# Performance work log

Measured on AMD Instinct MI355X. Metric: run time of the kernel, lower is better.

## Reference

```python
import jax, jax.numpy as jnp
import numpy as np

B, N_CLS, M_TIME, U_LAB = 1024, 96, 256, 40


def setup_inputs() -> dict:
    key = jax.random.key(0)
    k1, k2, k3 = jax.random.split(key, 3)
    logits = jax.random.normal(k1, (B, N_CLS, M_TIME), dtype=jnp.float32)
    # module treats inputs as per-timestep class probabilities (softmax output of CRNN)
    out_padded = jax.nn.softmax(logits, axis=1)
    label = jax.random.randint(k2, (B, U_LAB), 1, N_CLS, dtype=jnp.int32)  # 0 is blank
    unpadded_w = jax.random.randint(k3, (B,), 512, 4 * M_TIME + 1, dtype=jnp.int32)
    return {"out_padded": out_padded, "label": label, "unpadded_w": unpadded_w}


def _alpha(probs, lab, T, L):
    # probs: (M, N) time-major class probabilities; lab: (U,) label indices; T traced int.
    # Faithful to compute_alpha: per-timestep renormalization over [start, end),
    # recurrence computed for s in [start, L).
    M = probs.shape[0]
    s_idx = jnp.arange(L)
    i_idx = jnp.maximum((s_idx - 1) // 2, 0)
    is_odd = (s_idx % 2) == 1
    cls = jnp.where(is_odd, lab[i_idx], 0)  # blank = class 0 for even s
    # skip (a[t-1][s-2]) allowed only for odd s != 1 with non-repeated label
    skip = is_odd & (s_idx != 1) & (lab[i_idx] != lab[jnp.maximum(i_idx - 1, 0)])

    p0 = probs[0]
    row0 = jnp.zeros((L,), probs.dtype).at[0].set(p0[0]).at[1].set(p0[lab[0]])
    c0 = row0[0] + row0[1]
    row0 = jnp.where((s_idx < 2) & (c0 > 0), row0 / jnp.where(c0 > 0, c0, 1.0), row0)

    def step(prev, t):
        start = jnp.maximum(0, L - 2 * (T - t))
        end = jnp.minimum(2 * t + 2, L)
        pm1 = jnp.concatenate([jnp.zeros((1,), prev.dtype), prev[:-1]])
        pm2 = jnp.concatenate([jnp.zeros((2,), prev.dtype), prev[:-2]])
        val = (prev
               + jnp.where(s_idx > 0, pm1, 0.0)
               + jnp.where(skip, pm2, 0.0)) * probs[t, cls]
        val = jnp.where(s_idx >= start, val, 0.0)  # s < start stays zero
        nmask = (s_idx >= start) & (s_idx < end)
        c = jnp.sum(jnp.where(nmask, val, 0.0))
        val = jnp.where(nmask & (c > 0), val / jnp.where(c > 0, c, 1.0), val)
        return val, val

    _, rows = jax.lax.scan(step, row0, jnp.arange(1, M))
    a = jnp.concatenate([row0[None, :], rows], axis=0)  # (M, L)
    return jnp.where((jnp.arange(M) < T)[:, None], a, 0.0)  # rows >= T are zero


def _ctc_single(out_cw, lab, w):
    probs = out_cw.T  # (M, N): time x classes, as in torch.transpose(out, 1, 0)
    M = probs.shape[0]
    U = lab.shape[0]
    L = 2 * U + 1
    T = w // 4
    a = _alpha(probs, lab, T, L)
    # 'beta' faithful to source: alpha on CLASS-flipped probs (torch.fliplr on (T,N))
    # with reversed labels, then flipud+fliplr of the (T,L) result.
    b_raw = _alpha(probs[:, ::-1], lab[::-1], T, L)
    src = T - 1 - jnp.arange(M)
    valid = (src >= 0) & (src < M)
    b = jnp.where(valid[:, None], b_raw[jnp.clip(src, 0, M - 1)], 0.0)[:, ::-1]
    ab = a * b  # (M, L)
    s_idx = jnp.arange(L)
    cls = jnp.where((s_idx % 2) == 1, lab[jnp.maximum((s_idx - 1) // 2, 0)], 0)
    lh = jnp.sum(ab / probs[:, cls], axis=1)  # (M,)
    tmask = jnp.arange(M) < T
    return -jnp.sum(jnp.where(tmask, jnp.log(jnp.where(tmask, lh, 1.0)), 0.0))


def reference(out_padded, label, unpadded_w):
    losses = jax.vmap(_ctc_single)(out_padded, label, unpadded_w)  # (B,)
    return jnp.sum(losses)
```

## Files before the change

kernel.cpp:

```cpp
#include <hip/hip_runtime.h>
#include <cmath>

namespace {
constexpr int BN = 1024;
constexpr int NC = 96;
constexpr int MT = 256;
constexpr int UL = 40;
constexpr int LS = 81;
constexpr int PAIRS = 41;
constexpr int ROWS = 128;

template <int CTRL>
__device__ __forceinline__ float dppf(float v) {
  return __builtin_bit_cast(
      float, __builtin_amdgcn_update_dpp(0, __builtin_bit_cast(int, v), CTRL,
                                         0xf, 0xf, true));
}
__device__ __forceinline__ float rl63(float x) {
  return __builtin_bit_cast(
      float, __builtin_amdgcn_readlane(__builtin_bit_cast(int, x), 63));
}
__device__ __forceinline__ float wave_sum(float x) {
  x += dppf<0x111>(x);
  x += dppf<0x112>(x);
  x += dppf<0x114>(x);
  x += dppf<0x118>(x);
  x += dppf<0x142>(x);
  x += dppf<0x143>(x);
  return rl63(x);
}
__device__ __forceinline__ float wave_shr1(float v) { return dppf<0x138>(v); }
__device__ __forceinline__ float fast_rcp(float x) {
  return __builtin_amdgcn_rcpf(x);
}
__device__ __forceinline__ unsigned packu(float a, float b) {
  unsigned ua = __builtin_bit_cast(unsigned, a) >> 16;
  unsigned ub = __builtin_bit_cast(unsigned, b) & 0xffff0000u;
  return ua | ub;
}
__device__ __forceinline__ float bf_lo(unsigned u) {
  return __builtin_bit_cast(float, u << 16);
}
__device__ __forceinline__ float bf_hi(unsigned u) {
  return __builtin_bit_cast(float, u & 0xffff0000u);
}

constexpr float FQ = 1e8f;
constexpr float SEPS = 1e-30f;

__global__ __launch_bounds__(128) void ctc_fused_kernel(
    const float* __restrict__ gout, const int* __restrict__ glabel,
    const int* __restrict__ gw, float* __restrict__ loss_out) {
  __shared__ unsigned srows[2][ROWS * PAIRS];
  __shared__ float spart[2];
  const int b = blockIdx.x;
  const int ph = threadIdx.x >> 6;
  const int i = threadIdx.x & 63;
  const float* P = gout + (size_t)b * (NC * MT);
  const int* lab = glabel + b * UL;
  const int T = gw[b] >> 2;

  const int s0 = 2 * i, s1 = s0 + 1;
  const float h0f = (i <= 40) ? 1.f : 0.f;
  const float h1f = (i <= 39) ? 1.f : 0.f;
  const int iw = (i <= 40) ? i : 40;
  const bool act = (i <= 40);

  const float* pB;
  const float* pL;
  float mskf;
  int col;
  if (ph == 0) {
    const int li = (i < UL) ? lab[i] : 0;
    const int lm = (i >= 1 && i < UL) ? lab[i - 1] : 0;
    pB = P;
    pL = P + (size_t)li * MT;
    mskf = (i >= 1 && i <= 39 && li != lm) ? 1.f : 0.f;
    col = iw;
  } else {
    const int rli = (i < UL) ? lab[UL - 1 - i] : 0;
    const int rlm = (i >= 1 && i < UL) ? lab[UL - i] : 0;
    pB = P + (size_t)(NC - 1) * MT;
    pL = P + (size_t)(NC - 1 - rli) * MT;
    mskf = (i >= 1 && i <= 39 && rli != rlm) ? 1.f : 0.f;
    col = 40 - iw;
  }
  unsigned* mrow = srows[ph];
  const unsigned* orow = srows[1 - ph];

  float pbv[8], plv[8];
  float4 LA = *(const float4*)(pB + 0), LB = *(const float4*)(pB + 4);
  float4 MA = *(const float4*)(pL + 0), MB = *(const float4*)(pL + 4);
  pbv[0] = LA.x; pbv[1] = LA.y; pbv[2] = LA.z; pbv[3] = LA.w;
  pbv[4] = LB.x; pbv[5] = LB.y; pbv[6] = LB.z; pbv[7] = LB.w;
  plv[0] = MA.x; plv[1] = MA.y; plv[2] = MA.z; plv[3] = MA.w;
  plv[4] = MB.x; plv[5] = MB.y; plv[6] = MB.z; plv[7] = MB.w;
  LA = *(const float4*)(pB + 8); LB = *(const float4*)(pB + 12);
  MA = *(const float4*)(pL + 8); MB = *(const float4*)(pL + 12);

  float v0 = (i == 0) ? pbv[0] : 0.f;
  float v1 = (i == 0) ? plv[0] : 0.f;
  float ss = wave_sum(v0 + v1);
  float r0q = FQ * fast_rcp(fmaxf(ss, SEPS));
  float r1q = FQ * fast_rcp(fmaxf(ss * r0q, SEPS));
  float r2q = FQ * fast_rcp(fmaxf(ss * r0q * r1q, SEPS));

  float f0[8], f1[8], fs[8];
  fs[0] = ss;
  if (ph == 0) {
    f0[0] = (i == 0) ? 1.f : 0.f;
    f1[0] = f0[0];
  } else {
    f0[0] = v0;
    f1[0] = 0.f;
  }
  float acc = 0.f;

#define CTC_STEP(T_, K_)                                              \
  {                                                                   \
    float pm1 = wave_shr1(v1);                                        \
    if (ph == 1 && (K_) >= 1) f1[(K_)-1] = pm1;                       \
    const float rh0 = r0q * h0f, rh1 = r0q * h1f;                     \
    float u0 = v0 + pm1;                                              \
    float u1 = (v0 + v1) + pm1 * mskf;                                \
    const int start_ = LS - 2 * (T - (T_));                           \
    if (s0 < start_) u0 = 0.f;                                        \
    if (s1 < start_) u1 = 0.f;                                        \
    const float x0 = u0 * rh0, x1 = u1 * rh1;                         \
    float n0 = x0 * pbv[(K_)];                                        \
    float n1 = x1 * plv[(K_)];                                        \
    float ssn = wave_sum(n0 + n1);                                    \
    float rn = FQ * fast_rcp(fmaxf(ssn, SEPS) * r1q * r2q);           \
    rn = fminf(fmaxf(rn, 1e-20f), 1e20f);                             \
    r0q = r1q; r1q = r2q; r2q = rn;                                   \
    v0 = n0; v1 = n1;                                                 \
    fs[(K_)] = ssn;                                                   \
    if (ph == 0) { f0[(K_)] = x0; f1[(K_)] = x1; }                    \
    else { f0[(K_)] = n0; }                                           \
  }

#define CTC_PUB(T0_)                                                  \
  {                                                                   \
    if (ph == 1) f1[7] = wave_shr1(v1);                               \
    if (act && (T0_) < ROWS) {                                        \
      _Pragma("unroll")                                               \
      for (int k = 0; k < 8; ++k) {                                   \
        float inv = fast_rcp(fmaxf(fs[k], SEPS));                     \
        mrow[((T0_) + k) * PAIRS + col] =                             \
            packu(f0[k] * inv, f1[k] * inv);                          \
      }                                                               \
    }                                                                 \
  }

#define CTC_TERMS(T0_)                                                \
  if (2 * (T0_) >= T - 15) {                                          \
    __syncthreads();                                                  \
    _Pragma("unroll")                                                 \
    for (int kk = 0; kk < 8; ++kk) {                                  \
      const int k = (T0_) + kk;                                       \
      if (k < T) {                                                    \
        const int tb = T - 1 - k;                                     \
        const bool ck = (k + (T0_) >= T - 8);                         \
        const bool mine =                                             \
            (ph == 0) ? ck : (ck && (tb + (tb & ~7) < T - 8));        \
        if (mine) {                                                   \
          const unsigned av = orow[tb * PAIRS + col];                 \
          const float inv = fast_rcp(fmaxf(fs[kk], SEPS));            \
          const float pr =                                            \
              (bf_lo(av) * f0[kk] + bf_hi(av) * f1[kk]) * inv;        \
          const float d = wave_sum(pr);                               \
          acc += __logf(fmaxf(d, 1e-37f));                            \
        }                                                             \
      }                                                               \
    }                                                                 \
  }

#pragma unroll
  for (int k = 1; k < 8; ++k) CTC_STEP(k, k);
  CTC_PUB(0);

  for (int t0 = 8; t0 < T; t0 += 8) {
    pbv[0] = LA.x; pbv[1] = LA.y; pbv[2] = LA.z; pbv[3] = LA.w;
    pbv[4] = LB.x; pbv[5] = LB.y; pbv[6] = LB.z; pbv[7] = LB.w;
    plv[0] = MA.x; plv[1] = MA.y; plv[2] = MA.z; plv[3] = MA.w;
    plv[4] = MB.x; plv[5] = MB.y; plv[6] = MB.z; plv[7] = MB.w;
    int np = t0 + 8;
    if (np > 248) np = 248;
    LA = *(const float4*)(pB + np); LB = *(const float4*)(pB + np + 4);
    MA = *(const float4*)(pL + np); MB = *(const float4*)(pL + np + 4);
#pragma unroll
    for (int k = 0; k < 8; ++k) CTC_STEP(t0 + k, k);
    CTC_PUB(t0);
    CTC_TERMS(t0);
  }
#undef CTC_STEP
#undef CTC_PUB
#undef CTC_TERMS

  if (i == 0) spart[ph] = -acc;
  __syncthreads();
  if (threadIdx.x == 0) {
    float L = spart[0] + spart[1];
    loss_out[b] = fminf(fmaxf(L, -1e30f), 1e30f);
  }
}

__global__ void reduce_kernel(const float* __restrict__ loss_in,
                              float* __restrict__ out) {
  __shared__ double sm[256];
  const int tid = threadIdx.x;
  double s = 0.0;
  for (int k = tid; k < BN; k += 256) s += (double)loss_in[k];
  sm[tid] = s;
  __syncthreads();
  for (int w = 128; w >= 1; w >>= 1) {
    if (tid < w) sm[tid] += sm[tid + w];
    __syncthreads();
  }
  if (tid == 0) out[0] = (float)sm[0];
}
}

extern "C" void kernel_launch(void* const* d_in, const int* in_sizes, int n_in,
                              void* d_out, int out_size, void* d_ws, size_t ws_size,
                              hipStream_t stream) {
  const float* gout = (const float*)d_in[0];
  const int* glabel = (const int*)d_in[1];
  const int* gw = (const int*)d_in[2];
  float* loss = (float*)d_ws;
  ctc_fused_kernel<<<BN, 128, 0, stream>>>(gout, glabel, gw, loss);
  reduce_kernel<<<1, 256, 0, stream>>>(loss, (float*)d_out);
}
```

Measured before the change: 219.1 us.

## Run alpha and beta recurrences interleaved in a single wavefront per batch

Merges the two 64-thread waves (alpha and beta) into one wave that advances both recurrences in an interleaved loop, so their dependent DPP reductions and reciprocals can hide each other's latency. Block-level __syncthreads are removed because one wave owns both shared buffers. The term accumulation is rebalanced so each wave combines cross-products for k >= T/2 from both directions. The cost is doubled register pressure and serialised work per wave, with fewer threads per block to hide latency.

```diff
diff --git a/kernel.cpp b/kernel.cpp
--- a/kernel.cpp
+++ b/kernel.cpp
@@ -48,17 +48,17 @@
 constexpr float FQ = 1e8f;
 constexpr float SEPS = 1e-30f;
 
-__global__ __launch_bounds__(128) void ctc_fused_kernel(
+__global__ __launch_bounds__(64) void ctc_fused_kernel(
     const float* __restrict__ gout, const int* __restrict__ glabel,
     const int* __restrict__ gw, float* __restrict__ loss_out) {
-  __shared__ unsigned srows[2][ROWS * PAIRS];
-  __shared__ float spart[2];
+  __shared__ unsigned sA[ROWS * PAIRS];
+  __shared__ unsigned sB[ROWS * PAIRS];
   const int b = blockIdx.x;
-  const int ph = threadIdx.x >> 6;
-  const int i = threadIdx.x & 63;
+  const int i = threadIdx.x;
   const float* P = gout + (size_t)b * (NC * MT);
   const int* lab = glabel + b * UL;
   const int T = gw[b] >> 2;
+  const int kstart = T >> 1;
 
   const int s0 = 2 * i, s1 = s0 + 1;
   const float h0f = (i <= 40) ? 1.f : 0.f;
@@ -66,130 +66,151 @@
   const int iw = (i <= 40) ? i : 40;
   const bool act = (i <= 40);
 
-  const float* pB;
-  const float* pL;
-  float mskf;
-  int col;
-  if (ph == 0) {
-    const int li = (i < UL) ? lab[i] : 0;
-    const int lm = (i >= 1 && i < UL) ? lab[i - 1] : 0;
-    pB = P;
-    pL = P + (size_t)li * MT;
-    mskf = (i >= 1 && i <= 39 && li != lm) ? 1.f : 0.f;
-    col = iw;
-  } else {
-    const int rli = (i < UL) ? lab[UL - 1 - i] : 0;
-    const int rlm = (i >= 1 && i < UL) ? lab[UL - i] : 0;
-    pB = P + (size_t)(NC - 1) * MT;
-    pL = P + (size_t)(NC - 1 - rli) * MT;
-    mskf = (i >= 1 && i <= 39 && rli != rlm) ? 1.f : 0.f;
-    col = 40 - iw;
-  }
-  unsigned* mrow = srows[ph];
-  const unsigned* orow = srows[1 - ph];
-
-  float pbv[8], plv[8];
-  float4 LA = *(const float4*)(pB + 0), LB = *(const float4*)(pB + 4);
-  float4 MA = *(const float4*)(pL + 0), MB = *(const float4*)(pL + 4);
-  pbv[0] = LA.x; pbv[1] = LA.y; pbv[2] = LA.z; pbv[3] = LA.w;
-  pbv[4] = LB.x; pbv[5] = LB.y; pbv[6] = LB.z; pbv[7] = LB.w;
-  plv[0] = MA.x; plv[1] = MA.y; plv[2] = MA.z; plv[3] = MA.w;
-  plv[4] = MB.x; plv[5] = MB.y; plv[6] = MB.z; plv[7] = MB.w;
-  LA = *(const float4*)(pB + 8); LB = *(const float4*)(pB + 12);
-  MA = *(const float4*)(pL + 8); MB = *(const float4*)(pL + 12);
-
-  float v0 = (i == 0) ? pbv[0] : 0.f;
-  float v1 = (i == 0) ? plv[0] : 0.f;
-  float ss = wave_sum(v0 + v1);
-  float r0q = FQ * fast_rcp(fmaxf(ss, SEPS));
-  float r1q = FQ * fast_rcp(fmaxf(ss * r0q, SEPS));
-  float r2q = FQ * fast_rcp(fmaxf(ss * r0q * r1q, SEPS));
-
-  float f0[8], f1[8], fs[8];
-  fs[0] = ss;
-  if (ph == 0) {
-    f0[0] = (i == 0) ? 1.f : 0.f;
-    f1[0] = f0[0];
-  } else {
-    f0[0] = v0;
-    f1[0] = 0.f;
-  }
+  const int li = (i < UL) ? lab[i] : 0;
+  const int lm = (i >= 1 && i < UL) ? lab[i - 1] : 0;
+  const float* pBA = P;
+  const float* pLA = P + (size_t)li * MT;
+  const float mskA = (i >= 1 && i <= 39 && li != lm) ? 1.f : 0.f;
+  const int colA = iw;
+  const int rli = (i < UL) ? lab[UL - 1 - i] : 0;
+  const int rlm = (i >= 1 && i < UL) ? lab[UL - i] : 0;
+  const float* pBB = P + (size_t)(NC - 1) * MT;
+  const float* pLB = P + (size_t)(NC - 1 - rli) * MT;
+  const float mskB = (i >= 1 && i <= 39 && rli != rlm) ? 1.f : 0.f;
+  const int colB = 40 - iw;
+
+  float pbvA[8], plvA[8], pbvB[8], plvB[8];
+  float4 LAA = *(const float4*)(pBA + 0), LBA = *(const float4*)(pBA + 4);
+  float4 MAA = *(const float4*)(pLA + 0), MBA = *(const float4*)(pLA + 4);
+  float4 LAB = *(const float4*)(pBB + 0), LBB = *(const float4*)(pBB + 4);
+  float4 MAB = *(const float4*)(pLB + 0), MBB = *(const float4*)(pLB + 4);
+  pbvA[0] = LAA.x; pbvA[1] = LAA.y; pbvA[2] = LAA.z; pbvA[3] = LAA.w;
+  pbvA[4] = LBA.x; pbvA[5] = LBA.y; pbvA[6] = LBA.z; pbvA[7] = LBA.w;
+  plvA[0] = MAA.x; plvA[1] = MAA.y; plvA[2] = MAA.z; plvA[3] = MAA.w;
+  plvA[4] = MBA.x; plvA[5] = MBA.y; plvA[6] = MBA.z; plvA[7] = MBA.w;
+  pbvB[0] = LAB.x; pbvB[1] = LAB.y; pbvB[2] = LAB.z; pbvB[3] = LAB.w;
+  pbvB[4] = LBB.x; pbvB[5] = LBB.y; pbvB[6] = LBB.z; pbvB[7] = LBB.w;
+  plvB[0] = MAB.x; plvB[1] = MAB.y; plvB[2] = MAB.z; plvB[3] = MAB.w;
+  plvB[4] = MBB.x; plvB[5] = MBB.y; plvB[6] = MBB.z; plvB[7] = MBB.w;
+  LAA = *(const float4*)(pBA + 8); LBA = *(const float4*)(pBA + 12);
+  MAA = *(const float4*)(pLA + 8); MBA = *(const float4*)(pLA + 12);
+  LAB = *(const float4*)(pBB + 8); LBB = *(const float4*)(pBB + 12);
+  MAB = *(const float4*)(pLB + 8); MBB = *(const float4*)(pLB + 12);
+
+  float v0A = (i == 0) ? pbvA[0] : 0.f;
+  float v1A = (i == 0) ? plvA[0] : 0.f;
+  float v0B = (i == 0) ? pbvB[0] : 0.f;
+  float v1B = (i == 0) ? plvB[0] : 0.f;
+  float ssA = wave_sum(v0A + v1A);
+  float ssB = wave_sum(v0B + v1B);
+  float r0qA = FQ * fast_rcp(fmaxf(ssA, SEPS));
+  float r1qA = FQ * fast_rcp(fmaxf(ssA * r0qA, SEPS));
+  float r2qA = FQ * fast_rcp(fmaxf(ssA * r0qA * r1qA, SEPS));
+  float r0qB = FQ * fast_rcp(fmaxf(ssB, SEPS));
+  float r1qB = FQ * fast_rcp(fmaxf(ssB * r0qB, SEPS));
+  float r2qB = FQ * fast_rcp(fmaxf(ssB * r0qB * r1qB, SEPS));
+
+  float f0A[8], f1A[8], fsA[8];
+  float f0B[8], f1B[8], fsB[8];
+  fsA[0] = ssA;
+  f0A[0] = (i == 0) ? 1.f : 0.f;
+  f1A[0] = f0A[0];
+  fsB[0] = ssB;
+  f0B[0] = v0B;
+  f1B[0] = 0.f;
   float acc = 0.f;
 
-#define CTC_STEP(T_, K_)                                              \
+#define CTC_STEP(S, BETA, T_, K_)                                     \
   {                                                                   \
-    float pm1 = wave_shr1(v1);                                        \
-    if (ph == 1 && (K_) >= 1) f1[(K_)-1] = pm1;                       \
-    const float rh0 = r0q * h0f, rh1 = r0q * h1f;                     \
-    float u0 = v0 + pm1;                                              \
-    float u1 = (v0 + v1) + pm1 * mskf;                                \
+    float pm1 = wave_shr1(v1##S);                                     \
+    if ((BETA) && (K_) >= 1) f1##S[(K_)-1] = pm1;                     \
+    const float rh0 = r0q##S * h0f, rh1 = r0q##S * h1f;               \
+    float u0 = v0##S + pm1;                                           \
+    float u1 = (v0##S + v1##S) + pm1 * msk##S;                        \
     const int start_ = LS - 2 * (T - (T_));                           \
     if (s0 < start_) u0 = 0.f;                                        \
     if (s1 < start_) u1 = 0.f;                                        \
     const float x0 = u0 * rh0, x1 = u1 * rh1;                         \
-    float n0 = x0 * pbv[(K_)];                                        \
-    float n1 = x1 * plv[(K_)];                                        \
+    float n0 = x0 * pbv##S[(K_)];                                     \
+    float n1 = x1 * plv##S[(K_)];                                     \
     float ssn = wave_sum(n0 + n1);                                    \
-    float rn = FQ * fast_rcp(fmaxf(ssn, SEPS) * r1q * r2q);           \
+    float rn = FQ * fast_rcp(fmaxf(ssn, SEPS) * r1q##S * r2q##S);     \
     rn = fminf(fmaxf(rn, 1e-20f), 1e20f);                             \
-    r0q = r1q; r1q = r2q; r2q = rn;                                   \
-    v0 = n0; v1 = n1;                                                 \
-    fs[(K_)] = ssn;                                                   \
-    if (ph == 0) { f0[(K_)] = x0; f1[(K_)] = x1; }                    \
-    else { f0[(K_)] = n0; }                                           \
+    r0q##S = r1q##S; r1q##S = r2q##S; r2q##S = rn;                    \
+    v0##S = n0; v1##S = n1;                                           \
+    fs##S[(K_)] = ssn;                                                \
+    if (!(BETA)) { f0##S[(K_)] = x0; f1##S[(K_)] = x1; }              \
+    else { f0##S[(K_)] = n0; }                                        \
   }
 
 #define CTC_PUB(T0_)                                                  \
   {                                                                   \
-    if (ph == 1) f1[7] = wave_shr1(v1);                               \
-    if (act && (T0_) < ROWS) {                                        \
+    f1B[7] = wave_shr1(v1B);                                          \
+    if (act && (T0_)*2 < T) {                                         \
       _Pragma("unroll")                                               \
       for (int k = 0; k < 8; ++k) {                                   \
-        float inv = fast_rcp(fmaxf(fs[k], SEPS));                     \
-        mrow[((T0_) + k) * PAIRS + col] =                             \
-            packu(f0[k] * inv, f1[k] * inv);                          \
+        float invA_ = fast_rcp(fmaxf(fsA[k], SEPS));                  \
+        sA[((T0_) + k) * PAIRS + colA] =                              \
+            packu(f0A[k] * invA_, f1A[k] * invA_);                    \
+        float invB_ = fast_rcp(fmaxf(fsB[k], SEPS));                  \
+        sB[((T0_) + k) * PAIRS + colB] =                              \
+            packu(f0B[k] * invB_, f1B[k] * invB_);                    \
       }                                                               \
     }                                                                 \
   }
 
 #define CTC_TERMS(T0_)                                                \
-  if (2 * (T0_) >= T - 15) {                                          \
-    __syncthreads();                                                  \
+  if ((T0_) + 7 >= kstart) {                                          \
     _Pragma("unroll")                                                 \
     for (int kk = 0; kk < 8; ++kk) {                                  \
       const int k = (T0_) + kk;                                       \
-      if (k < T) {                                                    \
-        const int tb = T - 1 - k;                                     \
-        const bool ck = (k + (T0_) >= T - 8);                         \
-        const bool mine =                                             \
-            (ph == 0) ? ck : (ck && (tb + (tb & ~7) < T - 8));        \
-        if (mine) {                                                   \
-          const unsigned av = orow[tb * PAIRS + col];                 \
-          const float inv = fast_rcp(fmaxf(fs[kk], SEPS));            \
-          const float pr =                                            \
-              (bf_lo(av) * f0[kk] + bf_hi(av) * f1[kk]) * inv;        \
-          const float d = wave_sum(pr);                               \
-          acc += __logf(fmaxf(d, 1e-37f));                            \
+      if (k >= kstart && k < T) {                                     \
+        const int cross = T - 1 - k;                                  \
+        const float invA = fast_rcp(fmaxf(fsA[kk], SEPS));            \
+        const unsigned ub = sB[cross * PAIRS + iw];                   \
+        float prA =                                                   \
+            (bf_lo(ub) * f0A[kk] + bf_hi(ub) * f1A[kk]) * invA;       \
+        float dA = wave_sum(prA);                                     \
+        acc += __logf(fmaxf(dA, 1e-37f));                             \
+        if (2 * k != T - 1) {                                         \
+          const float invB = fast_rcp(fmaxf(fsB[kk], SEPS));          \
+          const unsigned ua = sA[cross * PAIRS + colB];               \
+          float prB =                                                 \
+              (bf_lo(ua) * f0B[kk] + bf_hi(ua) * f1B[kk]) * invB;     \
+          float dB = wave_sum(prB);                                   \
+          acc += __logf(fmaxf(dB, 1e-37f));                           \
         }                                                             \
       }                                                               \
     }                                                                 \
   }
 
 #pragma unroll
-  for (int k = 1; k < 8; ++k) CTC_STEP(k, k);
+  for (int k = 1; k < 8; ++k) {
+    CTC_STEP(A, 0, k, k);
+    CTC_STEP(B, 1, k, k);
+  }
   CTC_PUB(0);
 
   for (int t0 = 8; t0 < T; t0 += 8) {
-    pbv[0] = LA.x; pbv[1] = LA.y; pbv[2] = LA.z; pbv[3] = LA.w;
-    pbv[4] = LB.x; pbv[5] = LB.y; pbv[6] = LB.z; pbv[7] = LB.w;
-    plv[0] = MA.x; plv[1] = MA.y; plv[2] = MA.z; plv[3] = MA.w;
-    plv[4] = MB.x; plv[5] = MB.y; plv[6] = MB.z; plv[7] = MB.w;
+    pbvA[0] = LAA.x; pbvA[1] = LAA.y; pbvA[2] = LAA.z; pbvA[3] = LAA.w;
+    pbvA[4] = LBA.x; pbvA[5] = LBA.y; pbvA[6] = LBA.z; pbvA[7] = LBA.w;
+    plvA[0] = MAA.x; plvA[1] = MAA.y; plvA[2] = MAA.z; plvA[3] = MAA.w;
+    plvA[4] = MBA.x; plvA[5] = MBA.y; plvA[6] = MBA.z; plvA[7] = MBA.w;
+    pbvB[0] = LAB.x; pbvB[1] = LAB.y; pbvB[2] = LAB.z; pbvB[3] = LAB.w;
+    pbvB[4] = LBB.x; pbvB[5] = LBB.y; pbvB[6] = LBB.z; pbvB[7] = LBB.w;
+    plvB[0] = MAB.x; plvB[1] = MAB.y; plvB[2] = MAB.z; plvB[3] = MAB.w;
+    plvB[4] = MBB.x; plvB[5] = MBB.y; plvB[6] = MBB.z; plvB[7] = MBB.w;
     int np = t0 + 8;
     if (np > 248) np = 248;
-    LA = *(const float4*)(pB + np); LB = *(const float4*)(pB + np + 4);
-    MA = *(const float4*)(pL + np); MB = *(const float4*)(pL + np + 4);
+    LAA = *(const float4*)(pBA + np); LBA = *(const float4*)(pBA + np + 4);
+    MAA = *(const float4*)(pLA + np); MBA = *(const float4*)(pLA + np + 4);
+    LAB = *(const float4*)(pBB + np); LBB = *(const float4*)(pBB + np + 4);
+    MAB = *(const float4*)(pLB + np); MBB = *(const float4*)(pLB + np + 4);
 #pragma unroll
-    for (int k = 0; k < 8; ++k) CTC_STEP(t0 + k, k);
+    for (int k = 0; k < 8; ++k) {
+      CTC_STEP(A, 0, t0 + k, k);
+      CTC_STEP(B, 1, t0 + k, k);
+    }
     CTC_PUB(t0);
     CTC_TERMS(t0);
   }
@@ -197,10 +218,8 @@
 #undef CTC_PUB
 #undef CTC_TERMS
 
-  if (i == 0) spart[ph] = -acc;
-  __syncthreads();
-  if (threadIdx.x == 0) {
-    float L = spart[0] + spart[1];
+  if (i == 0) {
+    float L = -acc;
     loss_out[b] = fminf(fmaxf(L, -1e30f), 1e30f);
   }
 }
@@ -228,6 +247,6 @@
   const int* glabel = (const int*)d_in[1];
   const int* gw = (const int*)d_in[2];
   float* loss = (float*)d_ws;
-  ctc_fused_kernel<<<BN, 128, 0, stream>>>(gout, glabel, gw, loss);
+  ctc_fused_kernel<<<BN, 64, 0, stream>>>(gout, glabel, gw, loss);
   reduce_kernel<<<1, 256, 0, stream>>>(loss, (float*)d_out);
 }
```

Result: slower. 251.0 us (+14.6%).
